# Kernel optimization log

Hardware: AMD Instinct MI355X
Metric: run time of the kernel (lower is better)

## Reference

```python
import jax, jax.numpy as jnp
import numpy as np

C = 64
C8 = C // 8
N, H, W = 4, 512, 512


def conv1x1(x, w, b):
    # x: [N,C,H,W], w: [O,C], b: [O]
    return jnp.einsum('nchw,oc->nohw', x, w) + b[None, :, None, None]


def time_attention(x, qw, qb, kw, kb, vw, vb, gamma):
    # attention over the H axis; feature dim is (C//8)*W
    q = conv1x1(x, qw, qb)                     # [N,C8,H,W]
    k = conv1x1(x, kw, kb)                     # [N,C8,H,W]
    v = conv1x1(x, vw, vb)                     # [N,C,H,W]
    energy = jnp.einsum('nchw,ncgw->nhg', q, k)   # [N,H,H]
    attn = jax.nn.softmax(energy, axis=-1)
    out = jnp.einsum('ncgw,nhg->nchw', v, attn)   # [N,C,H,W]
    return gamma * out + x


def freq_attention(x, qw, qb, kw, kb, vw, vb, gamma):
    # attention over the W axis; feature dim is (C//8)*H
    q = conv1x1(x, qw, qb)
    k = conv1x1(x, kw, kb)
    v = conv1x1(x, vw, vb)
    energy = jnp.einsum('nchw,nchv->nwv', q, k)   # [N,W,W]
    attn = jax.nn.softmax(energy, axis=-1)
    out = jnp.einsum('nchv,nwv->nchw', v, attn)
    return gamma * out + x


def setup_inputs() -> dict:
    key = jax.random.key(0)
    ks = jax.random.split(key, 8)
    s = 0.05
    return {
        'x': jax.random.normal(ks[0], (N, C, H, W), dtype=jnp.float32),
        'tq_w': jax.random.normal(ks[1], (C8, C), dtype=jnp.float32) * s,
        'tq_b': jnp.zeros((C8,), jnp.float32),
        'tk_w': jax.random.normal(ks[2], (C8, C), dtype=jnp.float32) * s,
        'tk_b': jnp.zeros((C8,), jnp.float32),
        'tv_w': jax.random.normal(ks[3], (C, C), dtype=jnp.float32) * s,
        'tv_b': jnp.zeros((C,), jnp.float32),
        't_gamma': jnp.ones((1,), jnp.float32) * 0.5,
        'fq_w': jax.random.normal(ks[4], (C8, C), dtype=jnp.float32) * s,
        'fq_b': jnp.zeros((C8,), jnp.float32),
        'fk_w': jax.random.normal(ks[5], (C8, C), dtype=jnp.float32) * s,
        'fk_b': jnp.zeros((C8,), jnp.float32),
        'fv_w': jax.random.normal(ks[6], (C, C), dtype=jnp.float32) * s,
        'fv_b': jnp.zeros((C,), jnp.float32),
        'f_gamma': jnp.ones((1,), jnp.float32) * 0.5,
    }


def reference(x, tq_w, tq_b, tk_w, tk_b, tv_w, tv_b, t_gamma,
              fq_w, fq_b, fk_w, fk_b, fv_w, fv_b, f_gamma):
    t = time_attention(x, tq_w, tq_b, tk_w, tk_b, tv_w, tv_b, t_gamma)
    f = freq_attention(x, fq_w, fq_b, fk_w, fk_b, fv_w, fv_b, f_gamma)
    return x + t + f
```

## Files before the change

### kernel.cpp

```cpp
#include <hip/hip_runtime.h>
#include <stdint.h>

#define HW 262144
#define LDIM 512

typedef __bf16 bf16x8 __attribute__((ext_vector_type(8)));
typedef float f32x4 __attribute__((ext_vector_type(4)));
typedef short s16x8 __attribute__((ext_vector_type(8)));
typedef short s16x4 __attribute__((ext_vector_type(4)));

__device__ __forceinline__ unsigned short f2bf(float f) {
  union { float f; unsigned u; } v; v.f = f;
  unsigned r = v.u + 0x7fffu + ((v.u >> 16) & 1u);
  return (unsigned short)(r >> 16);
}

__device__ __forceinline__ float bf2f(short s) {
  union { unsigned u; float f; } v;
  v.u = ((unsigned)(unsigned short)s) << 16;
  return v.f;
}

__device__ __forceinline__ s16x8 pack_bf8(float4 a, float4 b) {
  s16x8 r;
  r[0] = (short)f2bf(a.x); r[1] = (short)f2bf(a.y);
  r[2] = (short)f2bf(a.z); r[3] = (short)f2bf(a.w);
  r[4] = (short)f2bf(b.x); r[5] = (short)f2bf(b.y);
  r[6] = (short)f2bf(b.z); r[7] = (short)f2bf(b.w);
  return r;
}

__device__ __forceinline__ f32x4 mfma16(bf16x8 a, bf16x8 b, f32x4 c) {
  return __builtin_amdgcn_mfma_f32_16x16x32_bf16(a, b, c, 0, 0, 0);
}

__device__ __forceinline__ void gl_lds16(const short* g, short* l) {
  __builtin_amdgcn_global_load_lds(
      (const __attribute__((address_space(1))) void*)g,
      (__attribute__((address_space(3))) void*)l, 16, 0, 0);
}

__global__ __launch_bounds__(256) void cast_k(const float* __restrict__ x,
                                              short* __restrict__ xb,
                                              short* __restrict__ xt) {
  __shared__ short L[64][72];
  int z = blockIdx.z;
  int h0 = blockIdx.y * 64, w0 = blockIdx.x * 64;
  int tid = threadIdx.x;
  size_t base = (size_t)z * HW;
  int hl = tid >> 4;
  int wl = (tid & 15) * 4;
#pragma unroll
  for (int it = 0; it < 4; ++it) {
    int h = h0 + hl + it * 16;
    float4 v = *(const float4*)(x + base + (size_t)h * 512 + w0 + wl);
    s16x4 b;
    b[0] = (short)f2bf(v.x); b[1] = (short)f2bf(v.y);
    b[2] = (short)f2bf(v.z); b[3] = (short)f2bf(v.w);
    *(s16x4*)(xb + base + (size_t)h * 512 + w0 + wl) = b;
    L[wl + 0][hl + it * 16] = b[0];
    L[wl + 1][hl + it * 16] = b[1];
    L[wl + 2][hl + it * 16] = b[2];
    L[wl + 3][hl + it * 16] = b[3];
  }
  __syncthreads();
#pragma unroll
  for (int it = 0; it < 4; ++it) {
    int w = hl + it * 16;
    s16x4 v = *(const s16x4*)(&L[w][wl]);
    *(s16x4*)(xt + base + (size_t)(w0 + w) * 512 + h0 + wl) = v;
  }
}

__global__ __launch_bounds__(256, 2) void conv_qkvf_k(
    const short* __restrict__ xb,
    const float* __restrict__ tqw, const float* __restrict__ tqb,
    const float* __restrict__ tkw, const float* __restrict__ tkb,
    const float* __restrict__ fqw, const float* __restrict__ fqb,
    const float* __restrict__ fkw, const float* __restrict__ fkb,
    const float* __restrict__ fvw,
    short* __restrict__ QT, short* __restrict__ KT,
    short* __restrict__ QF, short* __restrict__ KF,
    short* __restrict__ Vf) {
  __shared__ __align__(16) short As[128 * 72];
  __shared__ __align__(16) short Ws[96 * 72];
  __shared__ float bia[32];
  int tid = threadIdx.x;
  int n = blockIdx.x >> 11;
  int p0 = (blockIdx.x & 2047) << 7;
#pragma unroll
  for (int i = 0; i < 3; ++i) {
    int idx = i * 256 + tid;
    int co = idx >> 3, k0 = (idx & 7) * 8;
    const float* wrow = (co < 8)  ? tqw + co * 64
                      : (co < 16) ? tkw + (co - 8) * 64
                      : (co < 24) ? fqw + (co - 16) * 64
                      : (co < 32) ? fkw + (co - 24) * 64
                                  : fvw + (co - 32) * 64;
    float4 f0 = *(const float4*)(wrow + k0);
    float4 f1 = *(const float4*)(wrow + k0 + 4);
    *(s16x8*)(Ws + co * 72 + k0) = pack_bf8(f0, f1);
  }
  if (tid < 32) {
    const float* bsrc = (tid < 8) ? tqb : (tid < 16) ? tkb : (tid < 24) ? fqb : fkb;
    bia[tid] = bsrc[tid & 7];
  }
  {
    int mp = (tid & 31) * 4, k0 = (tid >> 5) * 8;
    const short* sp = xb + ((size_t)(n * 64 + k0)) * HW + p0 + mp;
    s16x8 t0, t1, t2, t3;
#pragma unroll
    for (int j = 0; j < 8; ++j) {
      s16x4 vv = *(const s16x4*)(sp + (size_t)j * HW);
      t0[j] = vv[0]; t1[j] = vv[1]; t2[j] = vv[2]; t3[j] = vv[3];
    }
    *(s16x8*)(As + (mp + 0) * 72 + k0) = t0;
    *(s16x8*)(As + (mp + 1) * 72 + k0) = t1;
    *(s16x8*)(As + (mp + 2) * 72 + k0) = t2;
    *(s16x8*)(As + (mp + 3) * 72 + k0) = t3;
  }
  __syncthreads();
  int lane = tid & 63, wv = tid >> 6, fr = lane & 15, q = lane >> 4;
  int wm = wv * 32;
  f32x4 acc[2][6];
#pragma unroll
  for (int mi = 0; mi < 2; ++mi)
#pragma unroll
    for (int ni = 0; ni < 6; ++ni) acc[mi][ni] = (f32x4){0.f, 0.f, 0.f, 0.f};
#pragma unroll
  for (int ks = 0; ks < 2; ++ks) {
    bf16x8 af[2], bw[6];
#pragma unroll
    for (int mi = 0; mi < 2; ++mi)
      af[mi] = *(const bf16x8*)(As + (wm + mi * 16 + fr) * 72 + ks * 32 + q * 8);
#pragma unroll
    for (int ni = 0; ni < 6; ++ni)
      bw[ni] = *(const bf16x8*)(Ws + (ni * 16 + fr) * 72 + ks * 32 + q * 8);
#pragma unroll
    for (int mi = 0; mi < 2; ++mi)
#pragma unroll
      for (int ni = 0; ni < 6; ++ni)
        acc[mi][ni] = mfma16(af[mi], bw[ni], acc[mi][ni]);
  }
#pragma unroll
  for (int mi = 0; mi < 2; ++mi)
#pragma unroll
    for (int ni = 0; ni < 6; ++ni) {
      int pl = wm + mi * 16 + q * 4;
      int co = ni * 16 + fr;
      float b = 0.f;
      short* dst;
      if (co < 32) {
        b = bia[co];
        short* dd = (co < 8) ? QT : (co < 16) ? KT : (co < 24) ? QF : KF;
        dst = dd + ((size_t)(n * 8 + (co & 7))) * HW;
      } else {
        dst = Vf + ((size_t)(n * 64 + (co - 32))) * HW;
      }
      s16x4 sv;
#pragma unroll
      for (int r = 0; r < 4; ++r) sv[r] = (short)f2bf(acc[mi][ni][r] + b);
      *(s16x4*)(dst + p0 + pl) = sv;
    }
}

__global__ __launch_bounds__(256, 2) void conv_v_k(
    const short* xin, const float* __restrict__ w64, short* vout) {
  __shared__ __align__(16) short As[128 * 72];
  __shared__ __align__(16) short Ws[64 * 72];
  int tid = threadIdx.x;
  int n = blockIdx.x >> 11;
  int p0 = (blockIdx.x & 2047) << 7;
#pragma unroll
  for (int i = 0; i < 2; ++i) {
    int idx = i * 256 + tid;
    int co = idx >> 3, k0 = (idx & 7) * 8;
    const float* wrow = w64 + co * 64;
    float4 f0 = *(const float4*)(wrow + k0);
    float4 f1 = *(const float4*)(wrow + k0 + 4);
    *(s16x8*)(Ws + co * 72 + k0) = pack_bf8(f0, f1);
  }
  {
    int mp = (tid & 31) * 4, k0 = (tid >> 5) * 8;
    const short* sp = xin + ((size_t)(n * 64 + k0)) * HW + p0 + mp;
    s16x8 t0, t1, t2, t3;
#pragma unroll
    for (int j = 0; j < 8; ++j) {
      s16x4 vv = *(const s16x4*)(sp + (size_t)j * HW);
      t0[j] = vv[0]; t1[j] = vv[1]; t2[j] = vv[2]; t3[j] = vv[3];
    }
    *(s16x8*)(As + (mp + 0) * 72 + k0) = t0;
    *(s16x8*)(As + (mp + 1) * 72 + k0) = t1;
    *(s16x8*)(As + (mp + 2) * 72 + k0) = t2;
    *(s16x8*)(As + (mp + 3) * 72 + k0) = t3;
  }
  __syncthreads();
  int lane = tid & 63, wv = tid >> 6, fr = lane & 15, q = lane >> 4;
  int wm = wv * 32;
  f32x4 acc[2][4];
#pragma unroll
  for (int mi = 0; mi < 2; ++mi)
#pragma unroll
    for (int ni = 0; ni < 4; ++ni) acc[mi][ni] = (f32x4){0.f, 0.f, 0.f, 0.f};
#pragma unroll
  for (int ks = 0; ks < 2; ++ks) {
    bf16x8 af[2], bw[4];
#pragma unroll
    for (int mi = 0; mi < 2; ++mi)
      af[mi] = *(const bf16x8*)(As + (wm + mi * 16 + fr) * 72 + ks * 32 + q * 8);
#pragma unroll
    for (int ni = 0; ni < 4; ++ni)
      bw[ni] = *(const bf16x8*)(Ws + (ni * 16 + fr) * 72 + ks * 32 + q * 8);
#pragma unroll
    for (int mi = 0; mi < 2; ++mi)
#pragma unroll
      for (int ni = 0; ni < 4; ++ni)
        acc[mi][ni] = mfma16(af[mi], bw[ni], acc[mi][ni]);
  }
#pragma unroll
  for (int mi = 0; mi < 2; ++mi)
#pragma unroll
    for (int ni = 0; ni < 4; ++ni) {
      int pl = wm + mi * 16 + q * 4;
      int co = ni * 16 + fr;
      short* d = vout + ((size_t)(n * 64 + co)) * HW + p0 + pl;
      s16x4 sv;
#pragma unroll
      for (int r = 0; r < 4; ++r) sv[r] = (short)f2bf(acc[mi][ni][r]);
      *(s16x4*)d = sv;
    }
}

template<bool OBF>
__global__ __launch_bounds__(256, 4) void gemm_a(
    const short* __restrict__ A0, long az, int zshA,
    const short* __restrict__ B0, long bz, int zshB,
    void* __restrict__ C0, long cz) {
  __shared__ __align__(16) short As[128 * 32];
  __shared__ __align__(16) short Bs[128 * 32];
  int tid = threadIdx.x;
  int z = blockIdx.z;
  int m0g = blockIdx.y * 128, n0g = blockIdx.x * 128;
  const short* Abz = A0 + (size_t)(z >> zshA) * (size_t)az;
  const short* Bbz = B0 + (size_t)(z >> zshB) * (size_t)bz;
  int lane = tid & 63, wv = tid >> 6;
  int wm = (wv >> 1) * 64, wn = (wv & 1) * 64;
  int fr = lane & 15, q = lane >> 4;

  int srow = lane >> 2;
  int sch = (lane & 3) * 8;
  const short* ga0 = Abz + (size_t)(m0g + wv * 32 + srow) * 512 + sch;
  const short* ga1 = ga0 + 16 * 512;
  const short* gb0 = Bbz + (size_t)(n0g + wv * 32 + srow) * 512 + sch;
  const short* gb1 = gb0 + 16 * 512;
  short* la0 = As + (wv * 32) * 32;
  short* la1 = As + (wv * 32 + 16) * 32;
  short* lb0 = Bs + (wv * 32) * 32;
  short* lb1 = Bs + (wv * 32 + 16) * 32;

  f32x4 acc[4][4];
#pragma unroll
  for (int mi = 0; mi < 4; ++mi)
#pragma unroll
    for (int ni = 0; ni < 4; ++ni) acc[mi][ni] = (f32x4){0.f, 0.f, 0.f, 0.f};

  for (int kk = 0; kk < 512; kk += 32) {
    gl_lds16(ga0 + kk, la0);
    gl_lds16(ga1 + kk, la1);
    gl_lds16(gb0 + kk, lb0);
    gl_lds16(gb1 + kk, lb1);
    __syncthreads();
    bf16x8 af[4], bg[4];
#pragma unroll
    for (int mi = 0; mi < 4; ++mi)
      af[mi] = *(const bf16x8*)(As + (wm + mi * 16 + fr) * 32 + q * 8);
#pragma unroll
    for (int ni = 0; ni < 4; ++ni)
      bg[ni] = *(const bf16x8*)(Bs + (wn + ni * 16 + fr) * 32 + q * 8);
#pragma unroll
    for (int mi = 0; mi < 4; ++mi)
#pragma unroll
      for (int ni = 0; ni < 4; ++ni)
        acc[mi][ni] = mfma16(af[mi], bg[ni], acc[mi][ni]);
    __syncthreads();
  }

  size_t coff = (size_t)z * (size_t)cz;
#pragma unroll
  for (int mi = 0; mi < 4; ++mi)
#pragma unroll
    for (int ni = 0; ni < 4; ++ni) {
      int row = m0g + wm + mi * 16 + q * 4;
      int col = n0g + wn + ni * 16 + fr;
#pragma unroll
      for (int r = 0; r < 4; ++r) {
        float v = acc[mi][ni][r];
        if constexpr (OBF) {
          ((short*)C0)[coff + (size_t)(row + r) * LDIM + col] = (short)f2bf(v);
        } else {
          ((float*)C0)[coff + (size_t)(row + r) * LDIM + col] = v;
        }
      }
    }
}

__global__ __launch_bounds__(256, 2) void gemm_t(
    const short* __restrict__ A0, long az,
    const short* __restrict__ B0, long bz,
    float* __restrict__ C0, long cz) {
  __shared__ __align__(16) short As[128 * 40];
  __shared__ __align__(16) short Bs[128 * 40];
  int tid = threadIdx.x;
  int z = blockIdx.z;
  int m0g = blockIdx.y * 128, n0g = blockIdx.x * 128;
  const short* Abz = A0 + (size_t)z * (size_t)az;
  const short* Bbz = B0 + (size_t)z * (size_t)bz;
  int lane = tid & 63, wv = tid >> 6;
  int wm = (wv >> 1) * 64, wn = (wv & 1) * 64;
  int fr = lane & 15, q = lane >> 4;
  int mp = (tid & 63) * 2, k0 = (tid >> 6) * 8;

  f32x4 acc[4][4];
#pragma unroll
  for (int mi = 0; mi < 4; ++mi)
#pragma unroll
    for (int ni = 0; ni < 4; ++ni) acc[mi][ni] = (f32x4){0.f, 0.f, 0.f, 0.f};

  for (int kk = 0; kk < 512; kk += 32) {
    {
      const short* s = Abz + (size_t)(kk + k0) * 512 + m0g + mp;
      s16x8 c0, c1;
#pragma unroll
      for (int j = 0; j < 8; ++j) {
        unsigned v = *(const unsigned*)(s + (size_t)j * 512);
        c0[j] = (short)(v & 0xffffu);
        c1[j] = (short)(v >> 16);
      }
      *(s16x8*)(As + mp * 40 + k0) = c0;
      *(s16x8*)(As + (mp + 1) * 40 + k0) = c1;
    }
    {
      const short* s = Bbz + (size_t)(kk + k0) * 512 + n0g + mp;
      s16x8 c0, c1;
#pragma unroll
      for (int j = 0; j < 8; ++j) {
        unsigned v = *(const unsigned*)(s + (size_t)j * 512);
        c0[j] = (short)(v & 0xffffu);
        c1[j] = (short)(v >> 16);
      }
      *(s16x8*)(Bs + mp * 40 + k0) = c0;
      *(s16x8*)(Bs + (mp + 1) * 40 + k0) = c1;
    }
    __syncthreads();
    bf16x8 af[4], bg[4];
#pragma unroll
    for (int mi = 0; mi < 4; ++mi)
      af[mi] = *(const bf16x8*)(As + (wm + mi * 16 + fr) * 40 + q * 8);
#pragma unroll
    for (int ni = 0; ni < 4; ++ni)
      bg[ni] = *(const bf16x8*)(Bs + (wn + ni * 16 + fr) * 40 + q * 8);
#pragma unroll
    for (int mi = 0; mi < 4; ++mi)
#pragma unroll
      for (int ni = 0; ni < 4; ++ni)
        acc[mi][ni] = mfma16(af[mi], bg[ni], acc[mi][ni]);
    __syncthreads();
  }

  size_t coff = (size_t)z * (size_t)cz;
#pragma unroll
  for (int mi = 0; mi < 4; ++mi)
#pragma unroll
    for (int ni = 0; ni < 4; ++ni) {
      int row = m0g + wm + mi * 16 + q * 4;
      int col = n0g + wn + ni * 16 + fr;
#pragma unroll
      for (int r = 0; r < 4; ++r)
        C0[coff + (size_t)(row + r) * LDIM + col] = acc[mi][ni][r];
    }
}

__global__ __launch_bounds__(256, 4) void softmax8_k(const float* __restrict__ Ep,
                                                     const float* __restrict__ gp,
                                                     short* __restrict__ A) {
  int tid = threadIdx.x;
  int lane = tid & 63, wv = tid >> 6;
  int row = blockIdx.x * 4 + wv;
  int n = row >> 9, h = row & 511;
  const float* base = Ep + (size_t)(n * 8) * HW + (size_t)h * 512 + lane * 8;
  float v[8] = {0.f, 0.f, 0.f, 0.f, 0.f, 0.f, 0.f, 0.f};
#pragma unroll
  for (int cc = 0; cc < 8; ++cc) {
    const float* e = base + (size_t)cc * HW;
    float4 a = *(const float4*)e;
    float4 b = *(const float4*)(e + 4);
    v[0] += a.x; v[1] += a.y; v[2] += a.z; v[3] += a.w;
    v[4] += b.x; v[5] += b.y; v[6] += b.z; v[7] += b.w;
  }
  float m = v[0];
#pragma unroll
  for (int j = 1; j < 8; ++j) m = fmaxf(m, v[j]);
#pragma unroll
  for (int off = 32; off >= 1; off >>= 1) m = fmaxf(m, __shfl_xor(m, off));
  float s = 0.f;
#pragma unroll
  for (int j = 0; j < 8; ++j) {
    v[j] = __expf(v[j] - m);
    s += v[j];
  }
#pragma unroll
  for (int off = 32; off >= 1; off >>= 1) s += __shfl_xor(s, off);
  float sc = gp[0] / s;
  s16x8 o;
#pragma unroll
  for (int j = 0; j < 8; ++j) o[j] = (short)f2bf(v[j] * sc);
  *(s16x8*)(A + (size_t)row * LDIM + lane * 8) = o;
}

__global__ __launch_bounds__(256, 3) void gemm_tf(
    const short* __restrict__ At, const short* __restrict__ Vt,
    const short* __restrict__ Vf, const short* __restrict__ Af,
    const short* __restrict__ xb,
    const float* __restrict__ tvb, const float* __restrict__ fvb,
    const float* __restrict__ tg, const float* __restrict__ fg,
    float* __restrict__ out) {
  __shared__ __align__(16) short As1[128 * 32];
  __shared__ __align__(16) short Bs1[128 * 32];
  __shared__ __align__(16) short As2[128 * 32];
  __shared__ __align__(16) short Bs2[128 * 32];
  int tid = threadIdx.x;
  int z = blockIdx.z;
  int n = z >> 6, o = z & 63;
  int m0g = blockIdx.y * 128, n0g = blockIdx.x * 128;
  const short* A1 = At + (size_t)n * HW;
  const short* B1 = Vt + (size_t)z * HW;
  const short* A2 = Vf + (size_t)z * HW;
  const short* B2 = Af + (size_t)n * HW;
  int lane = tid & 63, wv = tid >> 6;
  int wm = (wv >> 1) * 64, wn = (wv & 1) * 64;
  int fr = lane & 15, q = lane >> 4;

  int srow = lane >> 2;
  int sch = (lane & 3) * 8;
  const short* g1a = A1 + (size_t)(m0g + wv * 32 + srow) * 512 + sch;
  const short* g1b = B1 + (size_t)(n0g + wv * 32 + srow) * 512 + sch;
  const short* g2a = A2 + (size_t)(m0g + wv * 32 + srow) * 512 + sch;
  const short* g2b = B2 + (size_t)(n0g + wv * 32 + srow) * 512 + sch;
  short* l1a = As1 + (wv * 32) * 32;
  short* l1b = Bs1 + (wv * 32) * 32;
  short* l2a = As2 + (wv * 32) * 32;
  short* l2b = Bs2 + (wv * 32) * 32;

  f32x4 acc[4][4];
#pragma unroll
  for (int mi = 0; mi < 4; ++mi)
#pragma unroll
    for (int ni = 0; ni < 4; ++ni) acc[mi][ni] = (f32x4){0.f, 0.f, 0.f, 0.f};

  for (int kk = 0; kk < 512; kk += 32) {
    gl_lds16(g1a + kk, l1a);
    gl_lds16(g1a + kk + 16 * 512, l1a + 16 * 32);
    gl_lds16(g1b + kk, l1b);
    gl_lds16(g1b + kk + 16 * 512, l1b + 16 * 32);
    gl_lds16(g2a + kk, l2a);
    gl_lds16(g2a + kk + 16 * 512, l2a + 16 * 32);
    gl_lds16(g2b + kk, l2b);
    gl_lds16(g2b + kk + 16 * 512, l2b + 16 * 32);
    __syncthreads();
    {
      bf16x8 a1[4], b1[4];
#pragma unroll
      for (int mi = 0; mi < 4; ++mi)
        a1[mi] = *(const bf16x8*)(As1 + (wm + mi * 16 + fr) * 32 + q * 8);
#pragma unroll
      for (int ni = 0; ni < 4; ++ni)
        b1[ni] = *(const bf16x8*)(Bs1 + (wn + ni * 16 + fr) * 32 + q * 8);
#pragma unroll
      for (int mi = 0; mi < 4; ++mi)
#pragma unroll
        for (int ni = 0; ni < 4; ++ni)
          acc[mi][ni] = mfma16(a1[mi], b1[ni], acc[mi][ni]);
    }
    {
      bf16x8 a2[4], b2[4];
#pragma unroll
      for (int mi = 0; mi < 4; ++mi)
        a2[mi] = *(const bf16x8*)(As2 + (wm + mi * 16 + fr) * 32 + q * 8);
#pragma unroll
      for (int ni = 0; ni < 4; ++ni)
        b2[ni] = *(const bf16x8*)(Bs2 + (wn + ni * 16 + fr) * 32 + q * 8);
#pragma unroll
      for (int mi = 0; mi < 4; ++mi)
#pragma unroll
        for (int ni = 0; ni < 4; ++ni)
          acc[mi][ni] = mfma16(a2[mi], b2[ni], acc[mi][ni]);
    }
    __syncthreads();
  }

  float cb = tg[0] * tvb[o] + fg[0] * fvb[o];
  size_t zoff = (size_t)z * HW;
#pragma unroll
  for (int mi = 0; mi < 4; ++mi)
#pragma unroll
    for (int ni = 0; ni < 4; ++ni) {
      int row = m0g + wm + mi * 16 + q * 4;
      int col = n0g + wn + ni * 16 + fr;
#pragma unroll
      for (int r = 0; r < 4; ++r) {
        size_t idx = zoff + (size_t)(row + r) * LDIM + col;
        out[idx] = 3.f * bf2f(xb[idx]) + acc[mi][ni][r] + cb;
      }
    }
}

extern "C" void kernel_launch(void* const* d_in, const int* in_sizes, int n_in,
                              void* d_out, int out_size, void* d_ws, size_t ws_size,
                              hipStream_t stream) {
  (void)in_sizes; (void)n_in; (void)out_size;
  const float* x   = (const float*)d_in[0];
  const float* tqw = (const float*)d_in[1];
  const float* tqb = (const float*)d_in[2];
  const float* tkw = (const float*)d_in[3];
  const float* tkb = (const float*)d_in[4];
  const float* tvw = (const float*)d_in[5];
  const float* tvb = (const float*)d_in[6];
  const float* tg  = (const float*)d_in[7];
  const float* fqw = (const float*)d_in[8];
  const float* fqb = (const float*)d_in[9];
  const float* fkw = (const float*)d_in[10];
  const float* fkb = (const float*)d_in[11];
  const float* fvw = (const float*)d_in[12];
  const float* fvb = (const float*)d_in[13];
  const float* fg  = (const float*)d_in[14];
  float* out = (float*)d_out;

  const size_t per_n = ((size_t)64 * HW * 2) * 3
                     + ((size_t)8 * HW * 2) * 4;
  int nb = (ws_size >= 4 * per_n) ? 4
         : (ws_size >= 2 * per_n) ? 2 : 1;

  char* wb = (char*)d_ws;
  size_t sz_x  = (size_t)nb * 64 * HW * 2;
  size_t sz_qk = (size_t)nb * 8 * HW * 2;
  short* xb = (short*)(wb);
  short* xt = (short*)(wb + sz_x);
  short* Vf = (short*)(wb + 2 * sz_x);
  short* QT = (short*)(wb + 3 * sz_x);
  short* KT = (short*)(wb + 3 * sz_x + sz_qk);
  short* QF = (short*)(wb + 3 * sz_x + 2 * sz_qk);
  short* KF = (short*)(wb + 3 * sz_x + 3 * sz_qk);
  short* At = QT;
  short* Af = QF;

  for (int n0 = 0; n0 < 4; n0 += nb) {
    const float* xn = x + (size_t)n0 * 64 * HW;
    float* outn = out + (size_t)n0 * 64 * HW;
    float* EbT = outn;
    float* EbF = outn + (size_t)nb * 8 * HW;

    cast_k<<<dim3(8, 8, nb * 64), dim3(256), 0, stream>>>(xn, xb, xt);
    conv_qkvf_k<<<dim3(nb * 2048), dim3(256), 0, stream>>>(
        xb, tqw, tqb, tkw, tkb, fqw, fqb, fkw, fkb, fvw, QT, KT, QF, KF, Vf);
    conv_v_k<<<dim3(nb * 2048), dim3(256), 0, stream>>>(xt, tvw, xt);
    gemm_a<false><<<dim3(4, 4, nb * 8), dim3(256), 0, stream>>>(
        QT, (long)HW, 0, KT, (long)HW, 0, EbT, (long)HW);
    softmax8_k<<<dim3(nb * 128), dim3(256), 0, stream>>>(EbT, tg, At);
    gemm_t<<<dim3(4, 4, nb * 8), dim3(256), 0, stream>>>(
        QF, (long)HW, KF, (long)HW, EbF, (long)HW);
    softmax8_k<<<dim3(nb * 128), dim3(256), 0, stream>>>(EbF, fg, Af);
    gemm_tf<<<dim3(4, 4, nb * 64), dim3(256), 0, stream>>>(
        At, xt, Vf, Af, xb, tvb, fvb, tg, fg, outn);
  }
}
```

Before: 954.4 us.

## Fuse cast and all 1x1 convs into one kernel, transpose Vt in place

Removes the separate bf16 cast/transpose kernel and the second V conv. A single conv kernel now reads fp32 x directly, computes Q/K/Vt/Vf together, and an in-place tile-pair transpose kernel produces the transposed time V. The final GEMM now reads fp32 x for the residual instead of a bf16 copy. It halves its LDS by running the two GEMM phases sequentially with shared buffers, which allows higher occupancy. It also remaps block IDs to group tiles per XCD. Together these cut workspace traffic and one full pass over x, at the cost of an extra transpose pass over V and larger conv register pressure.

```diff
diff --git a/kernel.cpp b/kernel.cpp
--- a/kernel.cpp
+++ b/kernel.cpp
@@ -40,63 +40,32 @@
       (__attribute__((address_space(3))) void*)l, 16, 0, 0);
 }
 
-__global__ __launch_bounds__(256) void cast_k(const float* __restrict__ x,
-                                              short* __restrict__ xb,
-                                              short* __restrict__ xt) {
-  __shared__ short L[64][72];
-  int z = blockIdx.z;
-  int h0 = blockIdx.y * 64, w0 = blockIdx.x * 64;
-  int tid = threadIdx.x;
-  size_t base = (size_t)z * HW;
-  int hl = tid >> 4;
-  int wl = (tid & 15) * 4;
-#pragma unroll
-  for (int it = 0; it < 4; ++it) {
-    int h = h0 + hl + it * 16;
-    float4 v = *(const float4*)(x + base + (size_t)h * 512 + w0 + wl);
-    s16x4 b;
-    b[0] = (short)f2bf(v.x); b[1] = (short)f2bf(v.y);
-    b[2] = (short)f2bf(v.z); b[3] = (short)f2bf(v.w);
-    *(s16x4*)(xb + base + (size_t)h * 512 + w0 + wl) = b;
-    L[wl + 0][hl + it * 16] = b[0];
-    L[wl + 1][hl + it * 16] = b[1];
-    L[wl + 2][hl + it * 16] = b[2];
-    L[wl + 3][hl + it * 16] = b[3];
-  }
-  __syncthreads();
-#pragma unroll
-  for (int it = 0; it < 4; ++it) {
-    int w = hl + it * 16;
-    s16x4 v = *(const s16x4*)(&L[w][wl]);
-    *(s16x4*)(xt + base + (size_t)(w0 + w) * 512 + h0 + wl) = v;
-  }
-}
-
-__global__ __launch_bounds__(256, 2) void conv_qkvf_k(
-    const short* __restrict__ xb,
+__global__ __launch_bounds__(256, 2) void conv_all_k(
+    const float* __restrict__ x,
     const float* __restrict__ tqw, const float* __restrict__ tqb,
     const float* __restrict__ tkw, const float* __restrict__ tkb,
     const float* __restrict__ fqw, const float* __restrict__ fqb,
     const float* __restrict__ fkw, const float* __restrict__ fkb,
-    const float* __restrict__ fvw,
+    const float* __restrict__ tvw, const float* __restrict__ fvw,
     short* __restrict__ QT, short* __restrict__ KT,
     short* __restrict__ QF, short* __restrict__ KF,
-    short* __restrict__ Vf) {
+    short* __restrict__ Vt, short* __restrict__ Vf) {
   __shared__ __align__(16) short As[128 * 72];
-  __shared__ __align__(16) short Ws[96 * 72];
+  __shared__ __align__(16) short Ws[160 * 72];
   __shared__ float bia[32];
   int tid = threadIdx.x;
   int n = blockIdx.x >> 11;
   int p0 = (blockIdx.x & 2047) << 7;
 #pragma unroll
-  for (int i = 0; i < 3; ++i) {
+  for (int i = 0; i < 5; ++i) {
     int idx = i * 256 + tid;
     int co = idx >> 3, k0 = (idx & 7) * 8;
     const float* wrow = (co < 8)  ? tqw + co * 64
                       : (co < 16) ? tkw + (co - 8) * 64
                       : (co < 24) ? fqw + (co - 16) * 64
                       : (co < 32) ? fkw + (co - 24) * 64
-                                  : fvw + (co - 32) * 64;
+                      : (co < 96) ? tvw + (co - 32) * 64
+                                  : fvw + (co - 96) * 64;
     float4 f0 = *(const float4*)(wrow + k0);
     float4 f1 = *(const float4*)(wrow + k0 + 4);
     *(s16x8*)(Ws + co * 72 + k0) = pack_bf8(f0, f1);
@@ -107,12 +76,13 @@
   }
   {
     int mp = (tid & 31) * 4, k0 = (tid >> 5) * 8;
-    const short* sp = xb + ((size_t)(n * 64 + k0)) * HW + p0 + mp;
+    const float* sp = x + ((size_t)(n * 64 + k0)) * HW + p0 + mp;
     s16x8 t0, t1, t2, t3;
 #pragma unroll
     for (int j = 0; j < 8; ++j) {
-      s16x4 vv = *(const s16x4*)(sp + (size_t)j * HW);
-      t0[j] = vv[0]; t1[j] = vv[1]; t2[j] = vv[2]; t3[j] = vv[3];
+      float4 v = *(const float4*)(sp + (size_t)j * HW);
+      t0[j] = (short)f2bf(v.x); t1[j] = (short)f2bf(v.y);
+      t2[j] = (short)f2bf(v.z); t3[j] = (short)f2bf(v.w);
     }
     *(s16x8*)(As + (mp + 0) * 72 + k0) = t0;
     *(s16x8*)(As + (mp + 1) * 72 + k0) = t1;
@@ -122,40 +92,39 @@
   __syncthreads();
   int lane = tid & 63, wv = tid >> 6, fr = lane & 15, q = lane >> 4;
   int wm = wv * 32;
-  f32x4 acc[2][6];
+  f32x4 acc[2][10];
 #pragma unroll
   for (int mi = 0; mi < 2; ++mi)
 #pragma unroll
-    for (int ni = 0; ni < 6; ++ni) acc[mi][ni] = (f32x4){0.f, 0.f, 0.f, 0.f};
+    for (int ni = 0; ni < 10; ++ni) acc[mi][ni] = (f32x4){0.f, 0.f, 0.f, 0.f};
 #pragma unroll
   for (int ks = 0; ks < 2; ++ks) {
-    bf16x8 af[2], bw[6];
+    bf16x8 af[2];
 #pragma unroll
     for (int mi = 0; mi < 2; ++mi)
       af[mi] = *(const bf16x8*)(As + (wm + mi * 16 + fr) * 72 + ks * 32 + q * 8);
 #pragma unroll
-    for (int ni = 0; ni < 6; ++ni)
-      bw[ni] = *(const bf16x8*)(Ws + (ni * 16 + fr) * 72 + ks * 32 + q * 8);
-#pragma unroll
-    for (int mi = 0; mi < 2; ++mi)
-#pragma unroll
-      for (int ni = 0; ni < 6; ++ni)
-        acc[mi][ni] = mfma16(af[mi], bw[ni], acc[mi][ni]);
+    for (int ni = 0; ni < 10; ++ni) {
+      bf16x8 bw = *(const bf16x8*)(Ws + (ni * 16 + fr) * 72 + ks * 32 + q * 8);
+      acc[0][ni] = mfma16(af[0], bw, acc[0][ni]);
+      acc[1][ni] = mfma16(af[1], bw, acc[1][ni]);
+    }
   }
 #pragma unroll
   for (int mi = 0; mi < 2; ++mi)
 #pragma unroll
-    for (int ni = 0; ni < 6; ++ni) {
+    for (int ni = 0; ni < 10; ++ni) {
       int pl = wm + mi * 16 + q * 4;
       int co = ni * 16 + fr;
-      float b = 0.f;
+      float b = (co < 32) ? bia[co] : 0.f;
       short* dst;
       if (co < 32) {
-        b = bia[co];
         short* dd = (co < 8) ? QT : (co < 16) ? KT : (co < 24) ? QF : KF;
         dst = dd + ((size_t)(n * 8 + (co & 7))) * HW;
+      } else if (co < 96) {
+        dst = Vt + ((size_t)(n * 64 + (co - 32))) * HW;
       } else {
-        dst = Vf + ((size_t)(n * 64 + (co - 32))) * HW;
+        dst = Vf + ((size_t)(n * 64 + (co - 96))) * HW;
       }
       s16x4 sv;
 #pragma unroll
@@ -164,71 +133,38 @@
     }
 }
 
-__global__ __launch_bounds__(256, 2) void conv_v_k(
-    const short* xin, const float* __restrict__ w64, short* vout) {
-  __shared__ __align__(16) short As[128 * 72];
-  __shared__ __align__(16) short Ws[64 * 72];
+__global__ __launch_bounds__(256, 4) void trans_k(short* __restrict__ V) {
+  __shared__ short La[64][72];
+  __shared__ short Lb[64][72];
+  short* p = V + (size_t)blockIdx.y * HW;
+  int b = blockIdx.x;
+  int ti = 0;
+  while (b >= 8 - ti) { b -= 8 - ti; ++ti; }
+  int tj = ti + b;
   int tid = threadIdx.x;
-  int n = blockIdx.x >> 11;
-  int p0 = (blockIdx.x & 2047) << 7;
-#pragma unroll
-  for (int i = 0; i < 2; ++i) {
-    int idx = i * 256 + tid;
-    int co = idx >> 3, k0 = (idx & 7) * 8;
-    const float* wrow = w64 + co * 64;
-    float4 f0 = *(const float4*)(wrow + k0);
-    float4 f1 = *(const float4*)(wrow + k0 + 4);
-    *(s16x8*)(Ws + co * 72 + k0) = pack_bf8(f0, f1);
-  }
-  {
-    int mp = (tid & 31) * 4, k0 = (tid >> 5) * 8;
-    const short* sp = xin + ((size_t)(n * 64 + k0)) * HW + p0 + mp;
-    s16x8 t0, t1, t2, t3;
-#pragma unroll
-    for (int j = 0; j < 8; ++j) {
-      s16x4 vv = *(const s16x4*)(sp + (size_t)j * HW);
-      t0[j] = vv[0]; t1[j] = vv[1]; t2[j] = vv[2]; t3[j] = vv[3];
-    }
-    *(s16x8*)(As + (mp + 0) * 72 + k0) = t0;
-    *(s16x8*)(As + (mp + 1) * 72 + k0) = t1;
-    *(s16x8*)(As + (mp + 2) * 72 + k0) = t2;
-    *(s16x8*)(As + (mp + 3) * 72 + k0) = t3;
+  int hl = tid >> 4, wl = (tid & 15) * 4;
+#pragma unroll
+  for (int it = 0; it < 4; ++it) {
+    int r = hl + it * 16;
+    s16x4 va = *(const s16x4*)(p + (size_t)(ti * 64 + r) * 512 + tj * 64 + wl);
+    La[wl + 0][r] = va[0]; La[wl + 1][r] = va[1];
+    La[wl + 2][r] = va[2]; La[wl + 3][r] = va[3];
+    if (ti != tj) {
+      s16x4 vb = *(const s16x4*)(p + (size_t)(tj * 64 + r) * 512 + ti * 64 + wl);
+      Lb[wl + 0][r] = vb[0]; Lb[wl + 1][r] = vb[1];
+      Lb[wl + 2][r] = vb[2]; Lb[wl + 3][r] = vb[3];
+    }
   }
   __syncthreads();
-  int lane = tid & 63, wv = tid >> 6, fr = lane & 15, q = lane >> 4;
-  int wm = wv * 32;
-  f32x4 acc[2][4];
-#pragma unroll
-  for (int mi = 0; mi < 2; ++mi)
-#pragma unroll
-    for (int ni = 0; ni < 4; ++ni) acc[mi][ni] = (f32x4){0.f, 0.f, 0.f, 0.f};
-#pragma unroll
-  for (int ks = 0; ks < 2; ++ks) {
-    bf16x8 af[2], bw[4];
-#pragma unroll
-    for (int mi = 0; mi < 2; ++mi)
-      af[mi] = *(const bf16x8*)(As + (wm + mi * 16 + fr) * 72 + ks * 32 + q * 8);
-#pragma unroll
-    for (int ni = 0; ni < 4; ++ni)
-      bw[ni] = *(const bf16x8*)(Ws + (ni * 16 + fr) * 72 + ks * 32 + q * 8);
-#pragma unroll
-    for (int mi = 0; mi < 2; ++mi)
-#pragma unroll
-      for (int ni = 0; ni < 4; ++ni)
-        acc[mi][ni] = mfma16(af[mi], bw[ni], acc[mi][ni]);
-  }
-#pragma unroll
-  for (int mi = 0; mi < 2; ++mi)
-#pragma unroll
-    for (int ni = 0; ni < 4; ++ni) {
-      int pl = wm + mi * 16 + q * 4;
-      int co = ni * 16 + fr;
-      short* d = vout + ((size_t)(n * 64 + co)) * HW + p0 + pl;
-      s16x4 sv;
-#pragma unroll
-      for (int r = 0; r < 4; ++r) sv[r] = (short)f2bf(acc[mi][ni][r]);
-      *(s16x4*)d = sv;
-    }
+#pragma unroll
+  for (int it = 0; it < 4; ++it) {
+    int c = hl + it * 16;
+    *(s16x4*)(p + (size_t)(tj * 64 + c) * 512 + ti * 64 + wl) =
+        *(const s16x4*)(&La[c][wl]);
+    if (ti != tj)
+      *(s16x4*)(p + (size_t)(ti * 64 + c) * 512 + tj * 64 + wl) =
+          *(const s16x4*)(&Lb[c][wl]);
+  }
 }
 
 template<bool OBF>
@@ -417,39 +353,33 @@
   *(s16x8*)(A + (size_t)row * LDIM + lane * 8) = o;
 }
 
-__global__ __launch_bounds__(256, 3) void gemm_tf(
-    const short* __restrict__ At, const short* __restrict__ Vt,
+__global__ __launch_bounds__(256, 4) void gemm_tf(
+    const short* __restrict__ At, const short* __restrict__ VtT,
     const short* __restrict__ Vf, const short* __restrict__ Af,
-    const short* __restrict__ xb,
+    const float* __restrict__ x,
     const float* __restrict__ tvb, const float* __restrict__ fvb,
     const float* __restrict__ tg, const float* __restrict__ fg,
-    float* __restrict__ out) {
-  __shared__ __align__(16) short As1[128 * 32];
-  __shared__ __align__(16) short Bs1[128 * 32];
-  __shared__ __align__(16) short As2[128 * 32];
-  __shared__ __align__(16) short Bs2[128 * 32];
+    float* __restrict__ out, int Z) {
+  __shared__ __align__(16) short As[128 * 32];
+  __shared__ __align__(16) short Bs[128 * 32];
   int tid = threadIdx.x;
-  int z = blockIdx.z;
+  int f = blockIdx.x;
+  int xcd = f & 7, j = f >> 3;
+  int yt = j & 3;
+  int pid = xcd * (Z >> 1) + (j >> 2);
+  int nt = pid & 3, z = pid >> 2;
   int n = z >> 6, o = z & 63;
-  int m0g = blockIdx.y * 128, n0g = blockIdx.x * 128;
-  const short* A1 = At + (size_t)n * HW;
-  const short* B1 = Vt + (size_t)z * HW;
-  const short* A2 = Vf + (size_t)z * HW;
-  const short* B2 = Af + (size_t)n * HW;
+  int m0g = yt * 128, n0g = nt * 128;
+
   int lane = tid & 63, wv = tid >> 6;
   int wm = (wv >> 1) * 64, wn = (wv & 1) * 64;
   int fr = lane & 15, q = lane >> 4;
-
   int srow = lane >> 2;
   int sch = (lane & 3) * 8;
-  const short* g1a = A1 + (size_t)(m0g + wv * 32 + srow) * 512 + sch;
-  const short* g1b = B1 + (size_t)(n0g + wv * 32 + srow) * 512 + sch;
-  const short* g2a = A2 + (size_t)(m0g + wv * 32 + srow) * 512 + sch;
-  const short* g2b = B2 + (size_t)(n0g + wv * 32 + srow) * 512 + sch;
-  short* l1a = As1 + (wv * 32) * 32;
-  short* l1b = Bs1 + (wv * 32) * 32;
-  short* l2a = As2 + (wv * 32) * 32;
-  short* l2b = Bs2 + (wv * 32) * 32;
+  short* la0 = As + (wv * 32) * 32;
+  short* la1 = la0 + 16 * 32;
+  short* lb0 = Bs + (wv * 32) * 32;
+  short* lb1 = lb0 + 16 * 32;
 
   f32x4 acc[4][4];
 #pragma unroll
@@ -457,44 +387,48 @@
 #pragma unroll
     for (int ni = 0; ni < 4; ++ni) acc[mi][ni] = (f32x4){0.f, 0.f, 0.f, 0.f};
 
+  const short* g1a = At + (size_t)n * HW + (size_t)(m0g + wv * 32 + srow) * 512 + sch;
+  const short* g1b = VtT + (size_t)z * HW + (size_t)(n0g + wv * 32 + srow) * 512 + sch;
   for (int kk = 0; kk < 512; kk += 32) {
-    gl_lds16(g1a + kk, l1a);
-    gl_lds16(g1a + kk + 16 * 512, l1a + 16 * 32);
-    gl_lds16(g1b + kk, l1b);
-    gl_lds16(g1b + kk + 16 * 512, l1b + 16 * 32);
-    gl_lds16(g2a + kk, l2a);
-    gl_lds16(g2a + kk + 16 * 512, l2a + 16 * 32);
-    gl_lds16(g2b + kk, l2b);
-    gl_lds16(g2b + kk + 16 * 512, l2b + 16 * 32);
-    __syncthreads();
-    {
-      bf16x8 a1[4], b1[4];
-#pragma unroll
-      for (int mi = 0; mi < 4; ++mi)
-        a1[mi] = *(const bf16x8*)(As1 + (wm + mi * 16 + fr) * 32 + q * 8);
+    gl_lds16(g1a + kk, la0);
+    gl_lds16(g1a + kk + 16 * 512, la1);
+    gl_lds16(g1b + kk, lb0);
+    gl_lds16(g1b + kk + 16 * 512, lb1);
+    __syncthreads();
+    bf16x8 af[4], bg[4];
+#pragma unroll
+    for (int mi = 0; mi < 4; ++mi)
+      af[mi] = *(const bf16x8*)(As + (wm + mi * 16 + fr) * 32 + q * 8);
+#pragma unroll
+    for (int ni = 0; ni < 4; ++ni)
+      bg[ni] = *(const bf16x8*)(Bs + (wn + ni * 16 + fr) * 32 + q * 8);
+#pragma unroll
+    for (int mi = 0; mi < 4; ++mi)
 #pragma unroll
       for (int ni = 0; ni < 4; ++ni)
-        b1[ni] = *(const bf16x8*)(Bs1 + (wn + ni * 16 + fr) * 32 + q * 8);
-#pragma unroll
-      for (int mi = 0; mi < 4; ++mi)
-#pragma unroll
-        for (int ni = 0; ni < 4; ++ni)
-          acc[mi][ni] = mfma16(a1[mi], b1[ni], acc[mi][ni]);
-    }
-    {
-      bf16x8 a2[4], b2[4];
-#pragma unroll
-      for (int mi = 0; mi < 4; ++mi)
-        a2[mi] = *(const bf16x8*)(As2 + (wm + mi * 16 + fr) * 32 + q * 8);
+        acc[mi][ni] = mfma16(af[mi], bg[ni], acc[mi][ni]);
+    __syncthreads();
+  }
+  const short* g2a = Vf + (size_t)z * HW + (size_t)(m0g + wv * 32 + srow) * 512 + sch;
+  const short* g2b = Af + (size_t)n * HW + (size_t)(n0g + wv * 32 + srow) * 512 + sch;
+  for (int kk = 0; kk < 512; kk += 32) {
+    gl_lds16(g2a + kk, la0);
+    gl_lds16(g2a + kk + 16 * 512, la1);
+    gl_lds16(g2b + kk, lb0);
+    gl_lds16(g2b + kk + 16 * 512, lb1);
+    __syncthreads();
+    bf16x8 af[4], bg[4];
+#pragma unroll
+    for (int mi = 0; mi < 4; ++mi)
+      af[mi] = *(const bf16x8*)(As + (wm + mi * 16 + fr) * 32 + q * 8);
+#pragma unroll
+    for (int ni = 0; ni < 4; ++ni)
+      bg[ni] = *(const bf16x8*)(Bs + (wn + ni * 16 + fr) * 32 + q * 8);
+#pragma unroll
+    for (int mi = 0; mi < 4; ++mi)
 #pragma unroll
       for (int ni = 0; ni < 4; ++ni)
-        b2[ni] = *(const bf16x8*)(Bs2 + (wn + ni * 16 + fr) * 32 + q * 8);
-#pragma unroll
-      for (int mi = 0; mi < 4; ++mi)
-#pragma unroll
-        for (int ni = 0; ni < 4; ++ni)
-          acc[mi][ni] = mfma16(a2[mi], b2[ni], acc[mi][ni]);
-    }
+        acc[mi][ni] = mfma16(af[mi], bg[ni], acc[mi][ni]);
     __syncthreads();
   }
 
@@ -509,7 +443,7 @@
 #pragma unroll
       for (int r = 0; r < 4; ++r) {
         size_t idx = zoff + (size_t)(row + r) * LDIM + col;
-        out[idx] = 3.f * bf2f(xb[idx]) + acc[mi][ni][r] + cb;
+        out[idx] = 3.f * x[idx] + acc[mi][ni][r] + cb;
       }
     }
 }
@@ -535,21 +469,20 @@
   const float* fg  = (const float*)d_in[14];
   float* out = (float*)d_out;
 
-  const size_t per_n = ((size_t)64 * HW * 2) * 3
+  const size_t per_n = ((size_t)64 * HW * 2) * 2
                      + ((size_t)8 * HW * 2) * 4;
   int nb = (ws_size >= 4 * per_n) ? 4
          : (ws_size >= 2 * per_n) ? 2 : 1;
 
   char* wb = (char*)d_ws;
-  size_t sz_x  = (size_t)nb * 64 * HW * 2;
+  size_t sz_v  = (size_t)nb * 64 * HW * 2;
   size_t sz_qk = (size_t)nb * 8 * HW * 2;
-  short* xb = (short*)(wb);
-  short* xt = (short*)(wb + sz_x);
-  short* Vf = (short*)(wb + 2 * sz_x);
-  short* QT = (short*)(wb + 3 * sz_x);
-  short* KT = (short*)(wb + 3 * sz_x + sz_qk);
-  short* QF = (short*)(wb + 3 * sz_x + 2 * sz_qk);
-  short* KF = (short*)(wb + 3 * sz_x + 3 * sz_qk);
+  short* Vt = (short*)(wb);
+  short* Vf = (short*)(wb + sz_v);
+  short* QT = (short*)(wb + 2 * sz_v);
+  short* KT = (short*)(wb + 2 * sz_v + sz_qk);
+  short* QF = (short*)(wb + 2 * sz_v + 2 * sz_qk);
+  short* KF = (short*)(wb + 2 * sz_v + 3 * sz_qk);
   short* At = QT;
   short* Af = QF;
 
@@ -559,17 +492,17 @@
     float* EbT = outn;
     float* EbF = outn + (size_t)nb * 8 * HW;
 
-    cast_k<<<dim3(8, 8, nb * 64), dim3(256), 0, stream>>>(xn, xb, xt);
-    conv_qkvf_k<<<dim3(nb * 2048), dim3(256), 0, stream>>>(
-        xb, tqw, tqb, tkw, tkb, fqw, fqb, fkw, fkb, fvw, QT, KT, QF, KF, Vf);
-    conv_v_k<<<dim3(nb * 2048), dim3(256), 0, stream>>>(xt, tvw, xt);
+    conv_all_k<<<dim3(nb * 2048), dim3(256), 0, stream>>>(
+        xn, tqw, tqb, tkw, tkb, fqw, fqb, fkw, fkb, tvw, fvw,
+        QT, KT, QF, KF, Vt, Vf);
+    trans_k<<<dim3(36, nb * 64), dim3(256), 0, stream>>>(Vt);
     gemm_a<false><<<dim3(4, 4, nb * 8), dim3(256), 0, stream>>>(
         QT, (long)HW, 0, KT, (long)HW, 0, EbT, (long)HW);
     softmax8_k<<<dim3(nb * 128), dim3(256), 0, stream>>>(EbT, tg, At);
     gemm_t<<<dim3(4, 4, nb * 8), dim3(256), 0, stream>>>(
         QF, (long)HW, KF, (long)HW, EbF, (long)HW);
     softmax8_k<<<dim3(nb * 128), dim3(256), 0, stream>>>(EbF, fg, Af);
-    gemm_tf<<<dim3(4, 4, nb * 64), dim3(256), 0, stream>>>(
-        At, xt, Vf, Af, xb, tvb, fvb, tg, fg, outn);
-  }
-}
+    gemm_tf<<<dim3(16 * nb * 64), dim3(256), 0, stream>>>(
+        At, Vt, Vf, Af, xn, tvb, fvb, tg, fg, outn, nb * 64);
+  }
+}
```

Measured after the change: 952.5 us. About the same (-0.2%).
